# Optimization experiments

Hardware: AMD Instinct MI355X
Metric: run time of the kernel (lower is better)

The kernel has to match this reference:

```python
import jax, jax.numpy as jnp
import numpy as np

T, N = 64, 128          # temporal / spatial graph sizes; M = T*N product-graph nodes
B, F_IN, HID, F_OUT = 2, 32, 32, 16
L, K = 2, 4             # num_layers, filter order


def _sym_norm(key, n):
    # random symmetric adjacency, then D^{-1/2} A D^{-1/2} / 2 as in the torch __init__
    a = jax.random.uniform(key, (n, n), dtype=jnp.float32)
    a = 0.5 * (a + a.T)
    d = jnp.sum(a, axis=1)
    dinv = 1.0 / jnp.sqrt(d)
    return (dinv[:, None] * a * dinv[None, :]) * 0.5


def setup_inputs() -> dict:
    key = jax.random.key(0)
    ks = jax.random.split(key, 9)
    x = jax.random.normal(ks[0], (B, T * N, F_IN), dtype=jnp.float32)
    Adj_t = _sym_norm(ks[1], T)
    Adj_s = _sym_norm(ks[2], N)
    s = jax.random.normal(ks[3], (4,), dtype=jnp.float32) * 0.25
    H = jax.random.normal(ks[4], (L, K, HID, HID), dtype=jnp.float32) * 0.1
    W1 = jax.random.normal(ks[5], (F_IN, HID), dtype=jnp.float32) * (1.0 / np.sqrt(F_IN))
    b1 = jax.random.normal(ks[6], (HID,), dtype=jnp.float32) * 0.01
    W2 = jax.random.normal(ks[7], (HID, F_OUT), dtype=jnp.float32) * (1.0 / np.sqrt(HID))
    b2 = jax.random.normal(ks[8], (F_OUT,), dtype=jnp.float32) * 0.01
    return {"x": x, "Adj_t": Adj_t, "Adj_s": Adj_s, "s": s, "H": H,
            "W1": W1, "b1": b1, "W2": W2, "b2": b2}


def reference(x, Adj_t, Adj_s, s, H, W1, b1, W2, b2):
    t, n = Adj_t.shape[0], Adj_s.shape[0]
    I_t = jnp.eye(t, dtype=jnp.float32)
    I_s = jnp.eye(n, dtype=jnp.float32)
    # Adj = s0*I + s1*kron(I_t, Adj_s) + s2*kron(Adj_t, I_s) + s3*kron(Adj_t, Adj_s)
    Adj = (s[0] * jnp.eye(t * n, dtype=jnp.float32)
           + s[1] * jnp.kron(I_t, Adj_s)
           + s[2] * jnp.kron(Adj_t, I_s)
           + s[3] * jnp.kron(Adj_t, Adj_s))
    h = x @ W1 + b1                                   # [B, M, HID]
    num_layers = H.shape[0]
    for l in range(num_layers):
        Ah = jnp.einsum('mn,bnh->bmh', Adj, h)        # Adj @ x, hoisted out of k-loop
        # sum_k (Adj@x) @ H[l,k]  ==  einsum over k and h simultaneously
        h = jnp.tanh(jnp.einsum('bmh,khf->bmf', Ah, H[l]))
    return h @ W2 + b2                                # [B, M, F_OUT]
```

## Files before the change

### kernel.cpp

```cpp
#include <hip/hip_runtime.h>


__device__ __forceinline__ int swz(int row, int g) { return g ^ (row & 7); }

__device__ __forceinline__ float rlane(float v, int lane) {
    return __builtin_bit_cast(float, __builtin_amdgcn_readlane(__builtin_bit_cast(int, v), lane));
}

template<bool PROJ>
__global__ __launch_bounds__(512) void k_temporal(
    const float* __restrict__ src,
    const float* __restrict__ At,
    const float* __restrict__ W1, const float* __restrict__ b1,
    const float* __restrict__ s,
    float* __restrict__ up, float* __restrict__ pp)
{
    __shared__ float At_s[64 * 64];
    __shared__ float xs  [64 * 32];

    const int tid = threadIdx.x;
    const int b   = blockIdx.x >> 7;
    const int n   = blockIdx.x & 127;
    const int fg  = tid >> 6;
    const int lt  = tid & 63;

    const float s0v = s[0], s1v = s[1], s2v = s[2], s3v = s[3];

#pragma unroll
    for (int i = 0; i < 8; ++i) {
        int p = tid + 512 * i;
        int r = p >> 6, c = p & 63;
        At_s[r * 64 + (swz(r, c >> 2) << 2) + (c & 3)] = At[p];
    }

    float h0, h1, h2, h3;
    if (PROJ) {
        {
            int tt = tid >> 3, c4 = tid & 7;
            float4 v = *(const float4*)(src + ((size_t)(b * 8192 + tt * 128 + n)) * 32 + c4 * 4);
            *(float4*)&xs[tt * 32 + (swz(tt, c4) << 2)] = v;
        }
        float4 w1r = *(const float4*)(W1 + (lt & 31) * 32 + fg * 4);
        float4 bv  = *(const float4*)(b1 + fg * 4);
        __syncthreads();
        h0 = bv.x; h1 = bv.y; h2 = bv.z; h3 = bv.w;
#pragma unroll
        for (int k4 = 0; k4 < 8; ++k4) {
            float4 xv = *(const float4*)&xs[lt * 32 + (swz(lt, k4) << 2)];
#define PROJSTEP(a, k)                                   \
            h0 += (a) * rlane(w1r.x, (k));               \
            h1 += (a) * rlane(w1r.y, (k));               \
            h2 += (a) * rlane(w1r.z, (k));               \
            h3 += (a) * rlane(w1r.w, (k));
            PROJSTEP(xv.x, k4 * 4 + 0)
            PROJSTEP(xv.y, k4 * 4 + 1)
            PROJSTEP(xv.z, k4 * 4 + 2)
            PROJSTEP(xv.w, k4 * 4 + 3)
        }
    } else {
        float4 hv = *(const float4*)(src + (((size_t)(b * 128 + n)) * 64 + lt) * 32 + fg * 4);
        h0 = hv.x; h1 = hv.y; h2 = hv.z; h3 = hv.w;
        __syncthreads();
    }

    float w0 = 0.f, w1 = 0.f, w2 = 0.f, w3 = 0.f;
#pragma unroll
    for (int u4 = 0; u4 < 16; ++u4) {
        float4 av = *(const float4*)&At_s[lt * 64 + (swz(lt, u4) << 2)];
#define MIXSTEP(a, u)                                    \
        w0 += (a) * rlane(h0, (u));                      \
        w1 += (a) * rlane(h1, (u));                      \
        w2 += (a) * rlane(h2, (u));                      \
        w3 += (a) * rlane(h3, (u));
        MIXSTEP(av.x, u4 * 4 + 0)
        MIXSTEP(av.y, u4 * 4 + 1)
        MIXSTEP(av.z, u4 * 4 + 2)
        MIXSTEP(av.w, u4 * 4 + 3)
    }
    float4 uo, po;
    uo.x = s1v * h0 + s3v * w0;  po.x = s0v * h0 + s2v * w0;
    uo.y = s1v * h1 + s3v * w1;  po.y = s0v * h1 + s2v * w1;
    uo.z = s1v * h2 + s3v * w2;  po.z = s0v * h2 + s2v * w2;
    uo.w = s1v * h3 + s3v * w3;  po.w = s0v * h3 + s2v * w3;
    size_t base = ((size_t)((b * 64 + lt) * 128 + n)) * 32 + fg * 4;
    *(float4*)(up + base) = uo;
    *(float4*)(pp + base) = po;
}

template<bool LAST>
__global__ __launch_bounds__(512) void k_spatial(
    const float* __restrict__ up, const float* __restrict__ pp,
    const float* __restrict__ As, const float* __restrict__ H, int layer,
    const float* __restrict__ W2, const float* __restrict__ b2,
    float* __restrict__ hout, float* __restrict__ out)
{
    __shared__ float As_s[64 * 128];
    __shared__ float Ah_s[64 * 32];
    __shared__ float T_s [64 * 32];

    const int tid = threadIdx.x;
    const int b   = blockIdx.x >> 7;
    const int t   = (blockIdx.x >> 1) & 63;
    const int mh  = blockIdx.x & 1;
    const int fg  = tid >> 6;
    const int m   = tid & 63;

#pragma unroll
    for (int i = 0; i < 4; ++i) {
        int p = tid + 512 * i;
        int r = p >> 5, g = p & 31;
        float4 v = *(const float4*)(As + ((size_t)(mh * 64 + r)) * 128 + g * 4);
        *(float4*)&As_s[r * 128 + (swz(r, g) << 2)] = v;
    }
    const float* urow = up + ((size_t)(b * 64 + t)) * 4096;
    float4 ua = *(const float4*)(urow + (2 * m)     * 32 + fg * 4);
    float4 ub = *(const float4*)(urow + (2 * m + 1) * 32 + fg * 4);
    float4 hsr;
    {
        const float* Hl = H + layer * 4096 + (m & 31) * 32 + fg * 4;
        float4 q0 = *(const float4*)(Hl);
        float4 q1 = *(const float4*)(Hl + 1024);
        float4 q2 = *(const float4*)(Hl + 2048);
        float4 q3 = *(const float4*)(Hl + 3072);
        hsr.x = q0.x + q1.x + q2.x + q3.x;
        hsr.y = q0.y + q1.y + q2.y + q3.y;
        hsr.z = q0.z + q1.z + q2.z + q3.z;
        hsr.w = q0.w + q1.w + q2.w + q3.w;
    }
    float2 w2r, b2v;
    if (LAST) {
        w2r = *(const float2*)(W2 + (m & 31) * 16 + fg * 2);
        b2v = *(const float2*)(b2 + fg * 2);
    }
    float4 pv = *(const float4*)(pp + ((size_t)((b * 64 + t) * 128 + mh * 64 + m)) * 32 + fg * 4);
    float a0 = pv.x, a1 = pv.y, a2 = pv.z, a3 = pv.w;
    __syncthreads();

#pragma unroll
    for (int n4 = 0; n4 < 32; ++n4) {
        float4 av = *(const float4*)&As_s[m * 128 + (swz(m, n4) << 2)];
#define SPSTEP(a, reg, ln)                               \
        a0 += (a) * rlane(reg.x, (ln));                  \
        a1 += (a) * rlane(reg.y, (ln));                  \
        a2 += (a) * rlane(reg.z, (ln));                  \
        a3 += (a) * rlane(reg.w, (ln));
        SPSTEP(av.x, ua, 2 * n4)
        SPSTEP(av.y, ub, 2 * n4)
        SPSTEP(av.z, ua, 2 * n4 + 1)
        SPSTEP(av.w, ub, 2 * n4 + 1)
    }
    {
        float4 t4; t4.x = a0; t4.y = a1; t4.z = a2; t4.w = a3;
        *(float4*)&Ah_s[m * 32 + (swz(m, fg) << 2)] = t4;
    }
    __syncthreads();

    float c0 = 0.f, c1 = 0.f, c2 = 0.f, c3 = 0.f;
#pragma unroll
    for (int k4 = 0; k4 < 8; ++k4) {
        float4 av = *(const float4*)&Ah_s[m * 32 + (swz(m, k4) << 2)];
#define FSTEP(a, k)                                      \
        c0 += (a) * rlane(hsr.x, (k));                   \
        c1 += (a) * rlane(hsr.y, (k));                   \
        c2 += (a) * rlane(hsr.z, (k));                   \
        c3 += (a) * rlane(hsr.w, (k));
        FSTEP(av.x, k4 * 4 + 0)
        FSTEP(av.y, k4 * 4 + 1)
        FSTEP(av.z, k4 * 4 + 2)
        FSTEP(av.w, k4 * 4 + 3)
    }
    c0 = tanhf(c0); c1 = tanhf(c1); c2 = tanhf(c2); c3 = tanhf(c3);

    if (!LAST) {
        float4 o; o.x = c0; o.y = c1; o.z = c2; o.w = c3;
        *(float4*)(hout + (((size_t)(b * 128 + mh * 64 + m)) * 64 + t) * 32 + fg * 4) = o;
    } else {
        float4 t4; t4.x = c0; t4.y = c1; t4.z = c2; t4.w = c3;
        *(float4*)&T_s[m * 32 + (swz(m, fg) << 2)] = t4;
        __syncthreads();
        float o0 = b2v.x, o1 = b2v.y;
#pragma unroll
        for (int k4 = 0; k4 < 8; ++k4) {
            float4 tv = *(const float4*)&T_s[m * 32 + (swz(m, k4) << 2)];
#define OSTEP(a, k)                                      \
            o0 += (a) * rlane(w2r.x, (k));               \
            o1 += (a) * rlane(w2r.y, (k));
            OSTEP(tv.x, k4 * 4 + 0)
            OSTEP(tv.y, k4 * 4 + 1)
            OSTEP(tv.z, k4 * 4 + 2)
            OSTEP(tv.w, k4 * 4 + 3)
        }
        float2 o2; o2.x = o0; o2.y = o1;
        *(float2*)(out + ((size_t)((b * 64 + t) * 128 + mh * 64 + m)) * 16 + fg * 2) = o2;
    }
}

extern "C" void kernel_launch(void* const* d_in, const int* in_sizes, int n_in,
                              void* d_out, int out_size, void* d_ws, size_t ws_size,
                              hipStream_t stream)
{
    const float* x   = (const float*)d_in[0];
    const float* At  = (const float*)d_in[1];
    const float* As  = (const float*)d_in[2];
    const float* s   = (const float*)d_in[3];
    const float* H   = (const float*)d_in[4];
    const float* W1  = (const float*)d_in[5];
    const float* b1  = (const float*)d_in[6];
    const float* W2  = (const float*)d_in[7];
    const float* b2  = (const float*)d_in[8];
    float* out = (float*)d_out;

    float* up   = (float*)d_ws;
    float* pp   = up + 524288;
    float* hbuf = pp + 524288;

    k_temporal<true ><<<256, 512, 0, stream>>>(x,    At, W1, b1, s, up, pp);
    k_spatial <false><<<256, 512, 0, stream>>>(up, pp, As, H, 0, W2, b2, hbuf, out);
    k_temporal<false><<<256, 512, 0, stream>>>(hbuf, At, W1, b1, s, up, pp);
    k_spatial <true ><<<256, 512, 0, stream>>>(up, pp, As, H, 1, W2, b2, hbuf, out);
}
```

Baseline: 34.20 us.

## Split reduction dimension across two wave halves with 1024-thread blocks

Doubles block size to 1024 threads and splits the contraction loops (temporal mix over u, spatial mix over n) between two halves of waves. Partial sums are combined through a padded shared buffer. This halves the serial dependent FMA chain per wave, giving more latency hiding with only 256 blocks on the device. The cost is an extra LDS round trip and barrier, larger shared memory use, and some redundant compute in the upper half (projection, final matmuls).

```diff
diff --git a/kernel.cpp b/kernel.cpp
--- a/kernel.cpp
+++ b/kernel.cpp
@@ -8,7 +8,7 @@
 }
 
 template<bool PROJ>
-__global__ __launch_bounds__(512) void k_temporal(
+__global__ __launch_bounds__(1024) void k_temporal(
     const float* __restrict__ src,
     const float* __restrict__ At,
     const float* __restrict__ W1, const float* __restrict__ b1,
@@ -17,36 +17,40 @@
 {
     __shared__ float At_s[64 * 64];
     __shared__ float xs  [64 * 32];
-
-    const int tid = threadIdx.x;
-    const int b   = blockIdx.x >> 7;
-    const int n   = blockIdx.x & 127;
-    const int fg  = tid >> 6;
-    const int lt  = tid & 63;
+    __shared__ float part[2 * 64 * 36];
+
+    const int tid  = threadIdx.x;
+    const int b    = blockIdx.x >> 7;
+    const int n    = blockIdx.x & 127;
+    const int wave = tid >> 6;
+    const int fg   = wave & 7;
+    const int uh   = wave >> 3;
+    const int lane = tid & 63;
+    const int uhu  = __builtin_amdgcn_readfirstlane(uh);
 
     const float s0v = s[0], s1v = s[1], s2v = s[2], s3v = s[3];
 
 #pragma unroll
-    for (int i = 0; i < 8; ++i) {
-        int p = tid + 512 * i;
+    for (int i = 0; i < 4; ++i) {
+        int p = tid + 1024 * i;
         int r = p >> 6, c = p & 63;
         At_s[r * 64 + (swz(r, c >> 2) << 2) + (c & 3)] = At[p];
     }
 
     float h0, h1, h2, h3;
     if (PROJ) {
-        {
+        if (tid < 512) {
             int tt = tid >> 3, c4 = tid & 7;
             float4 v = *(const float4*)(src + ((size_t)(b * 8192 + tt * 128 + n)) * 32 + c4 * 4);
             *(float4*)&xs[tt * 32 + (swz(tt, c4) << 2)] = v;
         }
-        float4 w1r = *(const float4*)(W1 + (lt & 31) * 32 + fg * 4);
+        float4 w1r = *(const float4*)(W1 + (lane & 31) * 32 + fg * 4);
         float4 bv  = *(const float4*)(b1 + fg * 4);
         __syncthreads();
         h0 = bv.x; h1 = bv.y; h2 = bv.z; h3 = bv.w;
 #pragma unroll
         for (int k4 = 0; k4 < 8; ++k4) {
-            float4 xv = *(const float4*)&xs[lt * 32 + (swz(lt, k4) << 2)];
+            float4 xv = *(const float4*)&xs[lane * 32 + (swz(lane, k4) << 2)];
 #define PROJSTEP(a, k)                                   \
             h0 += (a) * rlane(w1r.x, (k));               \
             h1 += (a) * rlane(w1r.y, (k));               \
@@ -58,66 +62,83 @@
             PROJSTEP(xv.w, k4 * 4 + 3)
         }
     } else {
-        float4 hv = *(const float4*)(src + (((size_t)(b * 128 + n)) * 64 + lt) * 32 + fg * 4);
+        float4 hv = *(const float4*)(src + (((size_t)(b * 128 + n)) * 64 + lane) * 32 + fg * 4);
         h0 = hv.x; h1 = hv.y; h2 = hv.z; h3 = hv.w;
         __syncthreads();
     }
 
     float w0 = 0.f, w1 = 0.f, w2 = 0.f, w3 = 0.f;
 #pragma unroll
-    for (int u4 = 0; u4 < 16; ++u4) {
-        float4 av = *(const float4*)&At_s[lt * 64 + (swz(lt, u4) << 2)];
+    for (int i = 0; i < 8; ++i) {
+        int u4g = uhu * 8 + i;
+        float4 av = *(const float4*)&At_s[lane * 64 + (swz(lane, u4g) << 2)];
 #define MIXSTEP(a, u)                                    \
         w0 += (a) * rlane(h0, (u));                      \
         w1 += (a) * rlane(h1, (u));                      \
         w2 += (a) * rlane(h2, (u));                      \
         w3 += (a) * rlane(h3, (u));
-        MIXSTEP(av.x, u4 * 4 + 0)
-        MIXSTEP(av.y, u4 * 4 + 1)
-        MIXSTEP(av.z, u4 * 4 + 2)
-        MIXSTEP(av.w, u4 * 4 + 3)
-    }
-    float4 uo, po;
-    uo.x = s1v * h0 + s3v * w0;  po.x = s0v * h0 + s2v * w0;
-    uo.y = s1v * h1 + s3v * w1;  po.y = s0v * h1 + s2v * w1;
-    uo.z = s1v * h2 + s3v * w2;  po.z = s0v * h2 + s2v * w2;
-    uo.w = s1v * h3 + s3v * w3;  po.w = s0v * h3 + s2v * w3;
-    size_t base = ((size_t)((b * 64 + lt) * 128 + n)) * 32 + fg * 4;
-    *(float4*)(up + base) = uo;
-    *(float4*)(pp + base) = po;
+        MIXSTEP(av.x, uhu * 32 + i * 4 + 0)
+        MIXSTEP(av.y, uhu * 32 + i * 4 + 1)
+        MIXSTEP(av.z, uhu * 32 + i * 4 + 2)
+        MIXSTEP(av.w, uhu * 32 + i * 4 + 3)
+    }
+    {
+        float4 t4; t4.x = w0; t4.y = w1; t4.z = w2; t4.w = w3;
+        *(float4*)&part[(uh * 64 + lane) * 36 + fg * 4] = t4;
+    }
+    __syncthreads();
+
+    float4 p0 = *(const float4*)&part[lane * 36 + fg * 4];
+    float4 p1 = *(const float4*)&part[(64 + lane) * 36 + fg * 4];
+    float W0 = p0.x + p1.x, W1v = p0.y + p1.y, W2v = p0.z + p1.z, W3 = p0.w + p1.w;
+    size_t base = ((size_t)((b * 64 + lane) * 128 + n)) * 32 + fg * 4;
+    if (uh == 0) {
+        float4 uo;
+        uo.x = s1v * h0 + s3v * W0;  uo.y = s1v * h1 + s3v * W1v;
+        uo.z = s1v * h2 + s3v * W2v; uo.w = s1v * h3 + s3v * W3;
+        *(float4*)(up + base) = uo;
+    } else {
+        float4 po;
+        po.x = s0v * h0 + s2v * W0;  po.y = s0v * h1 + s2v * W1v;
+        po.z = s0v * h2 + s2v * W2v; po.w = s0v * h3 + s2v * W3;
+        *(float4*)(pp + base) = po;
+    }
 }
 
 template<bool LAST>
-__global__ __launch_bounds__(512) void k_spatial(
+__global__ __launch_bounds__(1024) void k_spatial(
     const float* __restrict__ up, const float* __restrict__ pp,
     const float* __restrict__ As, const float* __restrict__ H, int layer,
     const float* __restrict__ W2, const float* __restrict__ b2,
     float* __restrict__ hout, float* __restrict__ out)
 {
     __shared__ float As_s[64 * 128];
-    __shared__ float Ah_s[64 * 32];
-    __shared__ float T_s [64 * 32];
-
-    const int tid = threadIdx.x;
-    const int b   = blockIdx.x >> 7;
-    const int t   = (blockIdx.x >> 1) & 63;
-    const int mh  = blockIdx.x & 1;
-    const int fg  = tid >> 6;
-    const int m   = tid & 63;
-
-#pragma unroll
-    for (int i = 0; i < 4; ++i) {
-        int p = tid + 512 * i;
+    __shared__ float part[2 * 64 * 36];
+    __shared__ float T_s [64 * 36];
+
+    const int tid  = threadIdx.x;
+    const int b    = blockIdx.x >> 7;
+    const int t    = (blockIdx.x >> 1) & 63;
+    const int mh   = blockIdx.x & 1;
+    const int wave = tid >> 6;
+    const int fg   = wave & 7;
+    const int nh   = wave >> 3;
+    const int lane = tid & 63;
+    const int nhu  = __builtin_amdgcn_readfirstlane(nh);
+
+#pragma unroll
+    for (int i = 0; i < 2; ++i) {
+        int p = tid + 1024 * i;
         int r = p >> 5, g = p & 31;
         float4 v = *(const float4*)(As + ((size_t)(mh * 64 + r)) * 128 + g * 4);
         *(float4*)&As_s[r * 128 + (swz(r, g) << 2)] = v;
     }
     const float* urow = up + ((size_t)(b * 64 + t)) * 4096;
-    float4 ua = *(const float4*)(urow + (2 * m)     * 32 + fg * 4);
-    float4 ub = *(const float4*)(urow + (2 * m + 1) * 32 + fg * 4);
+    float4 ua = *(const float4*)(urow + (2 * lane)     * 32 + fg * 4);
+    float4 ub = *(const float4*)(urow + (2 * lane + 1) * 32 + fg * 4);
     float4 hsr;
     {
-        const float* Hl = H + layer * 4096 + (m & 31) * 32 + fg * 4;
+        const float* Hl = H + layer * 4096 + (lane & 31) * 32 + fg * 4;
         float4 q0 = *(const float4*)(Hl);
         float4 q1 = *(const float4*)(Hl + 1024);
         float4 q2 = *(const float4*)(Hl + 2048);
@@ -129,16 +150,20 @@
     }
     float2 w2r, b2v;
     if (LAST) {
-        w2r = *(const float2*)(W2 + (m & 31) * 16 + fg * 2);
+        w2r = *(const float2*)(W2 + (lane & 31) * 16 + fg * 2);
         b2v = *(const float2*)(b2 + fg * 2);
     }
-    float4 pv = *(const float4*)(pp + ((size_t)((b * 64 + t) * 128 + mh * 64 + m)) * 32 + fg * 4);
-    float a0 = pv.x, a1 = pv.y, a2 = pv.z, a3 = pv.w;
+    float4 pv = *(const float4*)(pp + ((size_t)((b * 64 + t) * 128 + mh * 64 + lane)) * 32 + fg * 4);
     __syncthreads();
 
-#pragma unroll
-    for (int n4 = 0; n4 < 32; ++n4) {
-        float4 av = *(const float4*)&As_s[m * 128 + (swz(m, n4) << 2)];
+    float a0, a1, a2, a3;
+    if (nh == 0) { a0 = pv.x; a1 = pv.y; a2 = pv.z; a3 = pv.w; }
+    else         { a0 = 0.f;  a1 = 0.f;  a2 = 0.f;  a3 = 0.f;  }
+
+#pragma unroll
+    for (int i = 0; i < 16; ++i) {
+        int n4 = nhu * 16 + i;
+        float4 av = *(const float4*)&As_s[lane * 128 + (swz(lane, n4) << 2)];
 #define SPSTEP(a, reg, ln)                               \
         a0 += (a) * rlane(reg.x, (ln));                  \
         a1 += (a) * rlane(reg.y, (ln));                  \
@@ -151,14 +176,18 @@
     }
     {
         float4 t4; t4.x = a0; t4.y = a1; t4.z = a2; t4.w = a3;
-        *(float4*)&Ah_s[m * 32 + (swz(m, fg) << 2)] = t4;
+        *(float4*)&part[(nh * 64 + lane) * 36 + fg * 4] = t4;
     }
     __syncthreads();
 
     float c0 = 0.f, c1 = 0.f, c2 = 0.f, c3 = 0.f;
 #pragma unroll
     for (int k4 = 0; k4 < 8; ++k4) {
-        float4 av = *(const float4*)&Ah_s[m * 32 + (swz(m, k4) << 2)];
+        float4 v0 = *(const float4*)&part[lane * 36 + k4 * 4];
+        float4 v1 = *(const float4*)&part[(64 + lane) * 36 + k4 * 4];
+        float4 av;
+        av.x = v0.x + v1.x; av.y = v0.y + v1.y;
+        av.z = v0.z + v1.z; av.w = v0.w + v1.w;
 #define FSTEP(a, k)                                      \
         c0 += (a) * rlane(hsr.x, (k));                   \
         c1 += (a) * rlane(hsr.y, (k));                   \
@@ -172,16 +201,20 @@
     c0 = tanhf(c0); c1 = tanhf(c1); c2 = tanhf(c2); c3 = tanhf(c3);
 
     if (!LAST) {
-        float4 o; o.x = c0; o.y = c1; o.z = c2; o.w = c3;
-        *(float4*)(hout + (((size_t)(b * 128 + mh * 64 + m)) * 64 + t) * 32 + fg * 4) = o;
+        if (nh == 0) {
+            float4 o; o.x = c0; o.y = c1; o.z = c2; o.w = c3;
+            *(float4*)(hout + (((size_t)(b * 128 + mh * 64 + lane)) * 64 + t) * 32 + fg * 4) = o;
+        }
     } else {
-        float4 t4; t4.x = c0; t4.y = c1; t4.z = c2; t4.w = c3;
-        *(float4*)&T_s[m * 32 + (swz(m, fg) << 2)] = t4;
+        if (nh == 0) {
+            float4 t4; t4.x = c0; t4.y = c1; t4.z = c2; t4.w = c3;
+            *(float4*)&T_s[lane * 36 + fg * 4] = t4;
+        }
         __syncthreads();
         float o0 = b2v.x, o1 = b2v.y;
 #pragma unroll
         for (int k4 = 0; k4 < 8; ++k4) {
-            float4 tv = *(const float4*)&T_s[m * 32 + (swz(m, k4) << 2)];
+            float4 tv = *(const float4*)&T_s[lane * 36 + k4 * 4];
 #define OSTEP(a, k)                                      \
             o0 += (a) * rlane(w2r.x, (k));               \
             o1 += (a) * rlane(w2r.y, (k));
@@ -190,8 +223,10 @@
             OSTEP(tv.z, k4 * 4 + 2)
             OSTEP(tv.w, k4 * 4 + 3)
         }
-        float2 o2; o2.x = o0; o2.y = o1;
-        *(float2*)(out + ((size_t)((b * 64 + t) * 128 + mh * 64 + m)) * 16 + fg * 2) = o2;
+        if (nh == 0) {
+            float2 o2; o2.x = o0; o2.y = o1;
+            *(float2*)(out + ((size_t)((b * 64 + t) * 128 + mh * 64 + lane)) * 16 + fg * 2) = o2;
+        }
     }
 }
 
@@ -214,8 +249,8 @@
     float* pp   = up + 524288;
     float* hbuf = pp + 524288;
 
-    k_temporal<true ><<<256, 512, 0, stream>>>(x,    At, W1, b1, s, up, pp);
-    k_spatial <false><<<256, 512, 0, stream>>>(up, pp, As, H, 0, W2, b2, hbuf, out);
-    k_temporal<false><<<256, 512, 0, stream>>>(hbuf, At, W1, b1, s, up, pp);
-    k_spatial <true ><<<256, 512, 0, stream>>>(up, pp, As, H, 1, W2, b2, hbuf, out);
-}
+    k_temporal<true ><<<256, 1024, 0, stream>>>(x,    At, W1, b1, s, up, pp);
+    k_spatial <false><<<256, 1024, 0, stream>>>(up, pp, As, H, 0, W2, b2, hbuf, out);
+    k_temporal<false><<<256, 1024, 0, stream>>>(hbuf, At, W1, b1, s, up, pp);
+    k_spatial <true ><<<256, 1024, 0, stream>>>(up, pp, As, H, 1, W2, b2, hbuf, out);
+}
```

Measured after the change: 48.38 us. 41.5% more time.
